# Kernel optimization log

Measured on AMD Instinct MI355X. Metric: run time of the kernel, lower is better.

The kernel has to match this reference:

```python
import jax, jax.numpy as jnp
import numpy as np

B = 1; C = 96; NH = 4; HD = 24; WIN = 3; LL = 27; SR = 8
Dd, Hh, Ww = 16, 40, 40
N = Dd * Hh * Ww
pH, pW, pD = Hh // SR, Ww // SR, Dd // SR
PL = pH * pW * pD
T = 4096


def _build_mask():
    p = WIN // 2
    m = np.zeros((Dd + 2 * p, Hh + 2 * p, Ww + 2 * p), bool)
    m[p:Dd + p, p:Hh + p, p:Ww + p] = True
    pats = np.stack([m[dz:dz + Dd, dy:dy + Hh, dx:dx + Ww]
                     for dz in range(WIN) for dy in range(WIN) for dx in range(WIN)], axis=-1)
    return jnp.asarray(~pats.reshape(N, LL))  # True where padded (masked)

MASK = _build_mask()


def _layernorm(x, w, b, eps=1e-5):
    mu = jnp.mean(x, axis=-1, keepdims=True)
    var = jnp.var(x, axis=-1, keepdims=True)
    return (x - mu) / jnp.sqrt(var + eps) * w + b


def _l2(x, eps=1e-12):
    n = jnp.sqrt(jnp.sum(x * x, axis=-1, keepdims=True))
    return x / jnp.maximum(n, eps)


def _unfold3d(x):
    # x: (B,C,D,H,W) -> (B,C,N,27), kernel order (kd,kh,kw) as torch unfold(2).unfold(3).unfold(4)
    p = WIN // 2
    xp = jnp.pad(x, ((0, 0), (0, 0), (p, p), (p, p), (p, p)))
    pats = [xp[:, :, dz:dz + Dd, dy:dy + Hh, dx:dx + Ww]
            for dz in range(WIN) for dy in range(WIN) for dx in range(WIN)]
    return jnp.stack(pats, axis=-1).reshape(x.shape[0], C, N, LL)


def _conv3(x, w):
    return jax.lax.conv_general_dilated(x, w, (1, 1, 1), 'SAME',
                                        dimension_numbers=('NCDHW', 'OIDHW', 'NCDHW'))


def _bn(x, p, eps=1e-5):
    sh = (1, C, 1, 1, 1)
    return (x - p[2].reshape(sh)) / jnp.sqrt(p[3].reshape(sh) + eps) * p[0].reshape(sh) + p[1].reshape(sh)


def _lrelu(x):
    return jnp.where(x >= 0, x, 0.01 * x)


def _resblock(x, w1, p1, w2, p2):
    h = _lrelu(_bn(_conv3(x, w1), p1))
    h = _bn(_conv3(h, w2), p2)
    return _lrelu(h + x)


def _forward(x, relative_pos_index, relative_coords_table, seq_length_scale,
             norm_w, norm_b, gamma, w_qkvv, temperature, temperature2, query_embedding,
             rel_bias_local, learnable_tokens, learnable_bias, sr_w, sr_b,
             epa_norm_w, epa_norm_b, w_kv, cpb1_w, cpb1_b, cpb2_w, cpb2_b,
             out1_w, out1_b, out2_w, out2_b,
             c51a_w, c51a_bn, c51b_w, c51b_bn, c52a_w, c52a_bn, c52b_w, c52b_bn,
             conv8_w, conv8_b):
    Bq = x.shape[0]
    # flatten (D,H,W) -> N tokens; pos_embed=True adds 1.0 (faithful to `x + True`)
    xt = x.reshape(Bq, C, N).transpose(0, 2, 1) + 1.0
    xn = _layernorm(xt, norm_w, norm_b)
    qkvv = (xn @ w_qkvv.T).reshape(Bq, N, 4, NH, HD).transpose(2, 0, 3, 1, 4)
    q, k, v_ca, v_sa = qkvv[0], qkvv[1], qkvv[2], qkvv[3]  # (B,NH,N,HD)
    qn = _l2(q)
    qs = (qn + query_embedding) * (jax.nn.softplus(temperature) * seq_length_scale)
    k_img = k.transpose(0, 1, 3, 2).reshape(Bq, C, Dd, Hh, Ww)
    v_img = v_sa.transpose(0, 1, 3, 2).reshape(Bq, C, Dd, Hh, Ww)
    k_loc = _unfold3d(k_img).reshape(Bq, NH, HD, N, LL).transpose(0, 1, 3, 2, 4)  # (B,NH,N,HD,LL)
    v_loc = _unfold3d(v_img).reshape(Bq, NH, HD, N, LL).transpose(0, 1, 3, 2, 4)
    a_loc = jnp.einsum('bhnd,bhndk->bhnk', qs, k_loc) + rel_bias_local[:, None, :]
    a_loc = jnp.where(MASK[None, None], -jnp.inf, a_loc)
    # pooled branch (note faithful (H,W,D) reshape as in source)
    xp = xn.transpose(0, 2, 1).reshape(Bq, C, Hh, Ww, Dd)
    xp = jax.nn.gelu(jnp.einsum('oc,bcxyz->boxyz', sr_w, xp)
                     + sr_b[None, :, None, None, None], approximate=False)
    xp = xp.reshape(Bq, C, pH, SR, pW, SR, pD, SR).mean(axis=(3, 5, 7))  # adaptive avg pool
    xp = xp.reshape(Bq, C, PL).transpose(0, 2, 1)
    xp = _layernorm(xp, epa_norm_w, epa_norm_b)
    kv = (xp @ w_kv.T).reshape(Bq, PL, 2 * NH, HD).transpose(0, 2, 1, 3)
    k_pool, v_pool = kv[:, :NH], kv[:, NH:]
    tab = jax.nn.relu(relative_coords_table @ cpb1_w.T + cpb1_b) @ cpb2_w.T + cpb2_b  # (T,NH)
    pool_bias = jnp.take(tab.T, relative_pos_index.reshape(-1), axis=1).reshape(NH, N, PL)
    a_pool = jnp.einsum('bhnd,bhpd->bhnp', qs, _l2(k_pool)) + pool_bias[None]
    attn = jax.nn.softmax(jnp.concatenate([a_loc, a_pool], axis=-1), axis=-1)
    a_loc, a_pool = attn[..., :LL], attn[..., LL:]
    a_loc = jnp.einsum('bhnd,hdk->bhnk', qn, learnable_tokens) + learnable_bias[None] + a_loc
    x_loc = jnp.einsum('bhnk,bhndk->bhnd', a_loc, v_loc)
    x_pool = jnp.einsum('bhnp,bhpd->bhnd', a_pool, v_pool)
    x_sa = (x_loc + x_pool).transpose(0, 2, 1, 3).reshape(Bq, N, C)
    # channel attention branch
    qt = _l2(q.transpose(0, 1, 3, 2))
    kt = _l2(k.transpose(0, 1, 3, 2))
    vt = v_ca.transpose(0, 1, 3, 2)
    a_ca = jax.nn.softmax(jnp.einsum('bhdn,bhen->bhde', qt, kt) * temperature2, axis=-1)
    x_ca = jnp.einsum('bhde,bhen->bhdn', a_ca, vt).transpose(0, 3, 1, 2).reshape(Bq, N, C)
    epa = jnp.concatenate([x_sa @ out1_w.T + out1_b, x_ca @ out2_w.T + out2_b], axis=-1)
    ax = xt + gamma * epa
    skip = ax.reshape(Bq, Hh, Ww, Dd, C).transpose(0, 4, 1, 2, 3)  # (B,C,H,W,D)
    h = _resblock(skip, c51a_w, c51a_bn, c51b_w, c51b_bn)
    h = _resblock(h, c52a_w, c52a_bn, c52b_w, c52b_bn)
    return skip + jnp.einsum('oc,bcxyz->boxyz', conv8_w, h) + conv8_b[None, :, None, None, None]


def setup_inputs():
    key = jax.random.key(0)
    ks = iter(jax.random.split(key, 64))
    r = lambda shape, s=0.02: jax.random.normal(next(ks), shape, jnp.float32) * s
    d = {}
    d['x'] = jax.random.normal(next(ks), (B, C, Dd, Hh, Ww), jnp.float32)
    d['relative_pos_index'] = jax.random.randint(next(ks), (N * PL,), 0, T, jnp.int32)
    d['relative_coords_table'] = jax.random.normal(next(ks), (T, 3), jnp.float32)
    d['seq_length_scale'] = jnp.ones((1,), jnp.float32)
    d['norm_w'] = 1.0 + r((C,)); d['norm_b'] = r((C,))
    d['gamma'] = jnp.full((C,), 0.01, jnp.float32)
    d['w_qkvv'] = r((4 * C, C))
    d['temperature'] = jnp.full((NH, 1, 1), float(np.log(np.exp(1 / 0.24) - 1)), jnp.float32)
    d['temperature2'] = jnp.ones((NH, 1, 1), jnp.float32)
    d['query_embedding'] = r((NH, 1, HD))
    d['rel_bias_local'] = r((NH, LL), 0.0004)
    d['learnable_tokens'] = r((NH, HD, LL))
    d['learnable_bias'] = jnp.zeros((NH, 1, LL), jnp.float32)
    d['sr_w'] = r((C, C)); d['sr_b'] = r((C,))
    d['epa_norm_w'] = 1.0 + r((C,)); d['epa_norm_b'] = r((C,))
    d['w_kv'] = r((2 * C, C))
    d['cpb1_w'] = r((512, 3)); d['cpb1_b'] = r((512,))
    d['cpb2_w'] = r((NH, 512)); d['cpb2_b'] = r((NH,))
    d['out1_w'] = r((C // 2, C)); d['out1_b'] = r((C // 2,))
    d['out2_w'] = r((C // 2, C)); d['out2_b'] = r((C // 2,))
    bn = lambda: jnp.stack([1.0 + r((C,)), r((C,)), jnp.zeros((C,), jnp.float32), jnp.ones((C,), jnp.float32)])
    d['c51a_w'] = r((C, C, 3, 3, 3)); d['c51a_bn'] = bn()
    d['c51b_w'] = r((C, C, 3, 3, 3)); d['c51b_bn'] = bn()
    d['c52a_w'] = r((C, C, 3, 3, 3)); d['c52a_bn'] = bn()
    d['c52b_w'] = r((C, C, 3, 3, 3)); d['c52b_bn'] = bn()
    d['conv8_w'] = r((C, C)); d['conv8_b'] = r((C,))
    return d


def reference(x, relative_pos_index, relative_coords_table, seq_length_scale,
              norm_w, norm_b, gamma, w_qkvv, temperature, temperature2, query_embedding,
              rel_bias_local, learnable_tokens, learnable_bias, sr_w, sr_b,
              epa_norm_w, epa_norm_b, w_kv, cpb1_w, cpb1_b, cpb2_w, cpb2_b,
              out1_w, out1_b, out2_w, out2_b,
              c51a_w, c51a_bn, c51b_w, c51b_bn, c52a_w, c52a_bn, c52b_w, c52b_bn,
              conv8_w, conv8_b):
    return _forward(x, relative_pos_index, relative_coords_table, seq_length_scale,
                    norm_w, norm_b, gamma, w_qkvv, temperature, temperature2, query_embedding,
                    rel_bias_local, learnable_tokens, learnable_bias, sr_w, sr_b,
                    epa_norm_w, epa_norm_b, w_kv, cpb1_w, cpb1_b, cpb2_w, cpb2_b,
                    out1_w, out1_b, out2_w, out2_b,
                    c51a_w, c51a_bn, c51b_w, c51b_bn, c52a_w, c52a_bn, c52b_w, c52b_bn,
                    conv8_w, conv8_b)
```

## Files before the change

kernel.cpp:

```cpp
#include <hip/hip_runtime.h>
#include <hip/hip_bf16.h>

#define NN 25600
#define CC 96
#define NHh 4
#define HDd 24
#define SSLOT 2457600
#define WP 269568

typedef unsigned short ushort_t;
typedef float f32x4 __attribute__((ext_vector_type(4)));
typedef short s16x8 __attribute__((ext_vector_type(8)));
typedef _Float16 f16;
typedef f16 h2v __attribute__((ext_vector_type(2)));

__device__ __forceinline__ float LD(const void* p, int i){
  return ((const float*)p)[i];
}
__device__ __forceinline__ float b2f(ushort_t u){ return __uint_as_float(((unsigned)u)<<16); }
__device__ __forceinline__ ushort_t f2b(float f){
  unsigned u = __float_as_uint(f);
  unsigned r = (u + 0x7fffu + ((u>>16)&1u))>>16;
  return (ushort_t)r;
}
__device__ __forceinline__ ushort_t f2h(float f){
  f16 hv = (f16)f;
  return *reinterpret_cast<ushort_t*>(&hv);
}
__device__ __forceinline__ float fdot2(h2v a, h2v b, float c){
#if __has_builtin(__builtin_amdgcn_fdot2)
  return __builtin_amdgcn_fdot2(a, b, c, false);
#else
  return c + (float)a[0]*(float)b[0] + (float)a[1]*(float)b[1];
#endif
}
__device__ __forceinline__ void gl_lds16(const void* g, const void* l){
  __builtin_amdgcn_global_load_lds(
      (const __attribute__((address_space(1))) unsigned*)g,
      (__attribute__((address_space(3))) unsigned*)l, 16, 0, 0);
}

#define NEGINF (-3.0e38f)

__global__ __launch_bounds__(256) void k_mega(
    const void* w0, const void* w1, const void* w2, const void* w3,
    const void* wq, const void* wsr, const void* w8,
    const void* o1w, const void* o1b, const void* o2w, const void* o2b,
    const void* b0, const void* b1, const void* b2bn, const void* b3,
    const void* ltok,
    ushort_t* __restrict__ WB2, ushort_t* __restrict__ WQH,
    ushort_t* __restrict__ WSH, ushort_t* __restrict__ W8H,
    ushort_t* __restrict__ WE, float* __restrict__ EB,
    float* __restrict__ BNS, ushort_t* __restrict__ LTOKT,
    float* __restrict__ ZB,
    const int* __restrict__ rpi, int* __restrict__ rpiT,
    const void* __restrict__ x, const void* __restrict__ nw,
    const void* __restrict__ nb, ushort_t* __restrict__ XNH,
    const void* __restrict__ rct, const void* __restrict__ w1t,
    const void* __restrict__ b1t, const void* __restrict__ w2t,
    const void* __restrict__ b2t, float* __restrict__ TAB)
{
  __shared__ __align__(16) char SMEM[15400];
  int b = blockIdx.x, tid = threadIdx.x;
  if(b < 4212){
    int e = b*256 + tid;
    {
      int t = e/WP, r = e%WP;
      int tap = r/9984, r2 = r%9984, o = r2/104, p = r2%104;
      const void* w = (t==0)? w0 : (t==1)? w1 : (t==2)? w2 : w3;
      WB2[e] = (p<96)? f2b(LD(w, (o*96+p)*27 + tap)) : (ushort_t)0;
    }
    if(e < 36864) WQH[e] = f2b(LD(wq,e));
    if(e < 9216){ WSH[e] = f2b(LD(wsr,e)); W8H[e] = f2b(LD(w8,e)); }
    if(e < 96*192){
      int o = e/192, c2 = e%192;
      float v = 0.f;
      if(o < 48 && c2 < 96)        v = LD(o1w, o*96 + c2);
      else if(o >= 48 && c2 >= 96) v = LD(o2w, (o-48)*96 + (c2-96));
      WE[e] = f2b(v);
      if(c2 == 0) EB[o] = (o<48)? LD(o1b,o) : LD(o2b,o-48);
    }
    if(e < 384){
      int t = e/96, o = e%96;
      const void* bn = (t==0)? b0 : (t==1)? b1 : (t==2)? b2bn : b3;
      float g=LD(bn,o), bb=LD(bn,96+o), mu=LD(bn,192+o), var=LD(bn,288+o);
      float s = g*rsqrtf(var+1e-5f);
      BNS[t*192+o] = s;
      BNS[t*192+96+o] = bb - mu*s;
    }
    if(e < 4096){
      int h = e/1024, r = e%1024, kk = r/32, d = r%32;
      float v = (d<24 && kk<27)? LD(ltok, (h*24+d)*27 + kk) : 0.f;
      LTOKT[e] = f2b(v);
    }
    if(e < 8) ZB[e] = 0.f;
  } else if(b < 4612){
    int* T = (int*)SMEM;
    int n0 = (b-4212)*64;
    for(int f=tid; f<3200; f+=256){
      int nl = f/50, p = f%50;
      T[p*65+nl] = rpi[n0*50 + f];
    }
    __syncthreads();
    for(int f=tid; f<3200; f+=256){
      int p = f>>6, nl = f&63;
      rpiT[(size_t)p*NN + n0 + nl] = T[p*65+nl];
    }
  } else if(b < 5012){
    float* reds  = (float*)SMEM;
    float* redss = reds + 256;
    ushort_t* OUT = (ushort_t*)(redss + 256);
    int bx = b - 4612;
    int nl = tid&63, cg = tid>>6;
    int n = bx*64 + nl;
    float v[24]; float s=0.f, ss=0.f;
    #pragma unroll
    for(int i=0;i<24;i++){
      float t = LD(x, (cg*24+i)*NN + n) + 1.0f;
      v[i]=t; s+=t; ss+=t*t;
    }
    reds[cg*64+nl]=s; redss[cg*64+nl]=ss;
    __syncthreads();
    float S  = reds[nl]+reds[64+nl]+reds[128+nl]+reds[192+nl];
    float SS = redss[nl]+redss[64+nl]+redss[128+nl]+redss[192+nl];
    float mu = S*(1.0f/CC);
    float inv = rsqrtf(SS*(1.0f/CC) - mu*mu + 1e-5f);
    #pragma unroll
    for(int i=0;i<24;i++){
      int c = cg*24+i;
      OUT[nl*100+c] = f2b((v[i]-mu)*inv*LD(nw,c) + LD(nb,c));
    }
    __syncthreads();
    for(int f=tid; f<3072; f+=256){
      int r = f/48, dp = f%48;
      unsigned pk = (unsigned)OUT[r*100+dp*2] | ((unsigned)OUT[r*100+dp*2+1]<<16);
      *reinterpret_cast<unsigned*>(XNH + (size_t)(bx*64+r)*96 + dp*2) = pk;
    }
  } else {
    float* red = (float*)SMEM;
    int tt = b - 5012, j = tid;
    float r0=LD(rct,tt*3), r1=LD(rct,tt*3+1), r2=LD(rct,tt*3+2);
    float hA = r0*LD(w1t,j*3) + r1*LD(w1t,j*3+1) + r2*LD(w1t,j*3+2) + LD(b1t,j);
    hA = fmaxf(hA, 0.f);
    int j2 = j + 256;
    float hB = r0*LD(w1t,j2*3) + r1*LD(w1t,j2*3+1) + r2*LD(w1t,j2*3+2) + LD(b1t,j2);
    hB = fmaxf(hB, 0.f);
    int lane=j&63, wid=j>>6;
    for(int h=0;h<4;h++){
      float v = hA*LD(w2t, h*512+j) + hB*LD(w2t, h*512+j2);
      #pragma unroll
      for(int off=32;off;off>>=1) v += __shfl_down(v, off);
      if(lane==0) red[wid*4+h]=v;
    }
    __syncthreads();
    if(j<4){
      float s = red[j] + red[4+j] + red[8+j] + red[12+j];
      TAB[tt*4+j] = s + LD(b2t,j);
    }
  }
}

__global__ __launch_bounds__(256,2) void k_qkvsr(
    const ushort_t* __restrict__ XNH, const ushort_t* __restrict__ WQH,
    const ushort_t* __restrict__ WSH, const void* __restrict__ srb,
    float* __restrict__ out, ushort_t* __restrict__ KH,
    ushort_t* __restrict__ VH, float* __restrict__ XP2){
  int tid=threadIdx.x, w=tid>>6, lane=tid&63, lan=lane&15, grp=lane>>4;
  int n = blockIdx.x*64 + w*16 + lan;
  const ushort_t* bp = XNH + n*96;
  if(blockIdx.y < 2){
    int ybase = blockIdx.y*192;
    f32x4 acc[12];
    #pragma unroll
    for(int mt=0;mt<12;mt++) acc[mt] = (f32x4)(0.f);
    #pragma unroll
    for(int s=0;s<3;s++){
      s16x8 b = *reinterpret_cast<const s16x8*>(bp + s*32 + grp*8);
      #pragma unroll
      for(int mt=0;mt<12;mt++){
        s16x8 a = *reinterpret_cast<const s16x8*>(WQH + (ybase+mt*16+lan)*96 + s*32 + grp*8);
        acc[mt] = __builtin_amdgcn_mfma_f32_16x16x32_bf16(a, b, acc[mt], 0,0,0);
      }
    }
    #pragma unroll
    for(int mt=0;mt<12;mt++){
      int o0 = ybase + mt*16 + grp*4;
      int sl = o0/96, rr = o0%96, h = rr/24, dd = rr%24;
      f32x4 v = acc[mt];
      if(sl == 3){
        ushort4 pk = { f2h(v[0]), f2h(v[1]), f2h(v[2]), f2h(v[3]) };
        *reinterpret_cast<ushort4*>(VH + ((size_t)h*NN+n)*24 + dd) = pk;
      } else {
        *reinterpret_cast<float4*>(out + sl*SSLOT + ((size_t)h*NN+n)*24 + dd) =
            (float4){v[0],v[1],v[2],v[3]};
        if(sl == 1){
          ushort4 pk = { f2h(v[0]), f2h(v[1]), f2h(v[2]), f2h(v[3]) };
          *reinterpret_cast<ushort4*>(KH + ((size_t)h*NN+n)*24 + dd) = pk;
        }
      }
    }
  } else {
    f32x4 acc[6];
    #pragma unroll
    for(int mt=0;mt<6;mt++) acc[mt] = (f32x4)(0.f);
    #pragma unroll
    for(int s=0;s<3;s++){
      s16x8 b = *reinterpret_cast<const s16x8*>(bp + s*32 + grp*8);
      #pragma unroll
      for(int mt=0;mt<6;mt++){
        s16x8 a = *reinterpret_cast<const s16x8*>(WSH + (mt*16+lan)*96 + s*32 + grp*8);
        acc[mt] = __builtin_amdgcn_mfma_f32_16x16x32_bf16(a, b, acc[mt], 0,0,0);
      }
    }
    #pragma unroll
    for(int mt=0;mt<6;mt++){
      #pragma unroll
      for(int r=0;r<4;r++){
        int o = mt*16 + grp*4 + r;
        float y = acc[mt][r] + LD(srb,o);
        y = 0.5f*y*(1.0f + erff(y*0.70710678118f));
        XP2[o*NN+n] = y;
      }
    }
  }
}

__global__ __launch_bounds__(256) void k_mid1(
    const float* __restrict__ Q, const void* __restrict__ temp,
    const void* __restrict__ sls, const void* __restrict__ qe,
    const ushort_t* __restrict__ LTOKT, const void* __restrict__ lbias,
    float* __restrict__ QS, ushort_t* __restrict__ LTH,
    const float* __restrict__ XP2, float* __restrict__ pooled)
{
  __shared__ ushort_t QL[4][64][32];
  int b = blockIdx.x, tid = threadIdx.x;
  if(b < 400){
    int h = tid>>6, nl = tid&63;
    int n0 = b*64, n = n0 + nl;
    const float* qr = Q + ((size_t)h*NN+n)*24;
    float qv[24]; float ssum=0.f;
    #pragma unroll
    for(int d=0;d<24;d++){ qv[d]=qr[d]; ssum+=qv[d]*qv[d]; }
    float inv = 1.0f/fmaxf(sqrtf(ssum), 1e-12f);
    float t = LD(temp,h);
    float sp = log1pf(expf(t)) * LD(sls,0);
    float* qs = QS + ((size_t)h*NN+n)*24;
    #pragma unroll
    for(int d=0;d<24;d+=2){
      float q0 = qv[d]*inv, q1 = qv[d+1]*inv;
      unsigned pk = (unsigned)f2b(q0) | ((unsigned)f2b(q1)<<16);
      *reinterpret_cast<unsigned*>(&QL[h][nl][d]) = pk;
      qs[d]   = (q0 + LD(qe, h*24+d))*sp;
      qs[d+1] = (q1 + LD(qe, h*24+d+1))*sp;
    }
    *reinterpret_cast<unsigned*>(&QL[h][nl][24]) = 0;
    *reinterpret_cast<unsigned*>(&QL[h][nl][26]) = 0;
    *reinterpret_cast<unsigned*>(&QL[h][nl][28]) = 0;
    *reinterpret_cast<unsigned*>(&QL[h][nl][30]) = 0;
    __syncthreads();
    int lane=tid&63, lan=lane&15, grp=lane>>4;
    f32x4 acc[4][2];
    #pragma unroll
    for(int j=0;j<4;j++)
      #pragma unroll
      for(int tt=0;tt<2;tt++) acc[j][tt] = (f32x4)(0.f);
    #pragma unroll
    for(int j=0;j<4;j++){
      s16x8 bb = *reinterpret_cast<const s16x8*>(&QL[h][j*16+lan][grp*8]);
      #pragma unroll
      for(int tt=0;tt<2;tt++){
        s16x8 a = *reinterpret_cast<const s16x8*>(LTOKT + h*1024 + (tt*16+lan)*32 + grp*8);
        acc[j][tt] = __builtin_amdgcn_mfma_f32_16x16x32_bf16(a, bb, acc[j][tt], 0,0,0);
      }
    }
    #pragma unroll
    for(int j=0;j<4;j++){
      int nn = n0 + j*16 + lan;
      #pragma unroll
      for(int tt=0;tt<2;tt++){
        int k0 = tt*16 + grp*4;
        if(k0 < 28){
          ushort4 pk;
          ushort_t* pp = reinterpret_cast<ushort_t*>(&pk);
          #pragma unroll
          for(int r=0;r<4;r++){
            int k = k0+r;
            float v = acc[j][tt][r] + ((k<27)? LD(lbias, h*27+k) : 0.f);
            pp[r] = f2h(v);
          }
          *reinterpret_cast<ushort4*>(LTH + ((size_t)h*NN+nn)*28 + k0) = pk;
        }
      }
    }
  } else {
    int w = tid>>6, lane = tid&63;
    int pb = (b-400)*4 + w;
    int c = pb % CC, p = pb / CC;
    int ph = p/10, pw = (p%10)/2, pd = p%2;
    float s = 0.f;
    for(int t=lane; t<512; t+=64){
      int i=t>>6, j=(t>>3)&7, k=t&7;
      int m = (ph*8+i)*640 + (pw*8+j)*16 + (pd*8+k);
      s += XP2[c*NN+m];
    }
    #pragma unroll
    for(int off=32;off;off>>=1) s += __shfl_down(s, off);
    if(lane==0) pooled[p*CC+c] = s*(1.0f/512.0f);
  }
}

__global__ void k_mid2(const float* __restrict__ pooled, const void* __restrict__ ew,
                       const void* __restrict__ eb, const void* __restrict__ wkv,
                       ushort_t* __restrict__ KPNH, ushort_t* __restrict__ VPH){
  __shared__ float row[96], lnr[96], st[2], kk[96];
  int p = blockIdx.x, t = threadIdx.x;
  if(t<96) row[t] = pooled[p*96+t];
  __syncthreads();
  if(t==0){
    float s=0.f, ss=0.f;
    for(int c=0;c<96;c++){ float v=row[c]; s+=v; ss+=v*v; }
    float mu=s*(1.0f/96.0f);
    float var=ss*(1.0f/96.0f)-mu*mu;
    st[0]=mu; st[1]=rsqrtf(var+1e-5f);
  }
  __syncthreads();
  if(t<96) lnr[t] = (row[t]-st[0])*st[1]*LD(ew,t) + LD(eb,t);
  __syncthreads();
  if(t<192){
    float a=0.f;
    for(int c=0;c<96;c++) a += LD(wkv, t*96+c)*lnr[c];
    int g=t/24, d=t%24;
    if(g<4) kk[t]=a;
    else    VPH[((g-4)*50+p)*24+d] = f2h(a);
  }
  __syncthreads();
  if(t<96){
    int g=t/24, d=t%24;
    float ss=0.f;
    #pragma unroll
    for(int e=0;e<24;e++){ float v=kk[g*24+e]; ss+=v*v; }
    float inv = 1.0f/fmaxf(sqrtf(ss),1e-12f);
    KPNH[((g*50+p)*24)+d] = f2h(kk[t]*inv);
  }
}

__global__ __launch_bounds__(512) void k_big(
    const float* __restrict__ QS, const ushort_t* __restrict__ KH,
    const ushort_t* __restrict__ VH,
    const ushort_t* __restrict__ KPNH, const ushort_t* __restrict__ VPH,
    const float* __restrict__ TAB, const int* __restrict__ rpiT,
    const void* __restrict__ rbl, const ushort_t* __restrict__ LTH,
    ushort_t* __restrict__ XH,
    const float* __restrict__ Q, const float* __restrict__ K,
    float* __restrict__ PAR)
{
  __shared__ ushort_t KVH[2][600*26];
  int bb = blockIdx.x, tid = threadIdx.x;
  if(bb < 400){
    int tile = bb % 100, h = bb / 100;
    int g = tile/25, sp = tile%25, hg = sp/5, wg = sp%5;
    int role = tid>>8, q = tid & 255;
    int wq = q>>6, l = q&63;
    int hy = l>>3, wx = l&7;
    int d0 = g*4 + wq;
    int h0 = hg*8+hy, w0 = wg*8+wx;
    int n = d0*1600 + h0*40 + w0;

    const ushort_t* KHh = KH + (size_t)h*NN*24;
    const ushort_t* VHh = VH + (size_t)h*NN*24;
    for(int f=tid; f<3600; f+=512){
      int t = f/1800, rem = f%1800, row = rem/3, qq = rem%3;
      int dr = row/100, yr = (row%100)/10, xr = row%10;
      int zc = min(max(g*4+dr-1,0),15), yc = min(max(hg*8+yr-1,0),39), xc = min(max(wg*8+xr-1,0),39);
      const ushort_t* src = (t? VHh : KHh) + (size_t)(zc*1600+yc*40+xc)*24 + qq*8;
      const unsigned* s32 = reinterpret_cast<const unsigned*>(src);
      unsigned a0=s32[0], a1=s32[1], a2=s32[2], a3=s32[3];
      unsigned* d32 = reinterpret_cast<unsigned*>(&KVH[t][row*26 + qq*8]);
      d32[0]=a0; d32[1]=a1; d32[2]=a2; d32[3]=a3;
    }

    h2v qp[12];
    {
      const float* qsp = QS + ((size_t)h*NN+n)*24;
      #pragma unroll
      for(int d=0; d<24; d+=4){
        float4 a = *reinterpret_cast<const float4*>(qsp+d);
        qp[d/2]   = (h2v){ (f16)a.x, (f16)a.y };
        qp[d/2+1] = (h2v){ (f16)a.z, (f16)a.w };
      }
    }
    __syncthreads();

    float m_r, s_r;
    h2v accA[12], accT[12];
    #pragma unroll
    for(int j=0;j<12;j++){ accA[j]=(h2v){(f16)0.f,(f16)0.f}; accT[j]=(h2v){(f16)0.f,(f16)0.f}; }

    const h2v* kph = reinterpret_cast<const h2v*>(KPNH) + (size_t)h*50*12;
    const h2v* vph = reinterpret_cast<const h2v*>(VPH)  + (size_t)h*50*12;

    if(role==0){
      float av[39]; unsigned okm=0;
      #pragma unroll
      for(int k=0;k<27;k++){
        int kz=k/9, ky=(k%9)/3, kx=k%3;
        bool ok = (unsigned)(d0+kz-1)<16u && (unsigned)(h0+ky-1)<40u && (unsigned)(w0+kx-1)<40u;
        float sc = NEGINF;
        if(ok){
          okm |= 1u<<k;
          const h2v* kr = reinterpret_cast<const h2v*>(
              &KVH[0][((wq+kz)*100 + (hy+ky)*10 + (wx+kx))*26]);
          sc = LD(rbl, h*27+k);
          #pragma unroll
          for(int j=0;j<12;j++) sc = fdot2(kr[j], qp[j], sc);
        }
        av[k]=sc;
      }
      #pragma unroll
      for(int p=0;p<12;p++){
        float sc = TAB[rpiT[(size_t)p*NN+n]*4 + h];
        const h2v* kr = kph + p*12;
        #pragma unroll
        for(int j=0;j<12;j++) sc = fdot2(kr[j], qp[j], sc);
        av[27+p]=sc;
      }
      float m = av[0];
      #pragma unroll
      for(int k=1;k<39;k++) m = fmaxf(m, av[k]);
      const f16* ltp = reinterpret_cast<const f16*>(LTH) + ((size_t)h*NN+n)*28;
      float s = 0.f;
      #pragma unroll
      for(int k=0;k<27;k++){
        if(okm>>k & 1u){
          int kz=k/9, ky=(k%9)/3, kx=k%3;
          float e = __expf(av[k]-m);
          s += e;
          float ltv = (float)ltp[k];
          h2v we = { (f16)e, (f16)e };
          h2v wt = { (f16)ltv, (f16)ltv };
          const h2v* vr = reinterpret_cast<const h2v*>(
              &KVH[1][((wq+kz)*100 + (hy+ky)*10 + (wx+kx))*26]);
          #pragma unroll
          for(int j=0;j<12;j++){
            accA[j] = vr[j]*we + accA[j];
            accT[j] = vr[j]*wt + accT[j];
          }
        }
      }
      #pragma unroll
      for(int p=0;p<12;p++){
        float e = __expf(av[27+p]-m);
        s += e;
        h2v we = { (f16)e, (f16)e };
        const h2v* vr = vph + p*12;
        #pragma unroll
        for(int j=0;j<12;j++) accA[j] = vr[j]*we + accA[j];
      }
      m_r = m; s_r = s;
    } else {
      float av[38];
      #pragma unroll
      for(int p=0;p<38;p++){
        int pp = p+12;
        float sc = TAB[rpiT[(size_t)pp*NN+n]*4 + h];
        const h2v* kr = kph + pp*12;
        #pragma unroll
        for(int j=0;j<12;j++) sc = fdot2(kr[j], qp[j], sc);
        av[p]=sc;
      }
      float m = av[0];
      #pragma unroll
      for(int p=1;p<38;p++) m = fmaxf(m, av[p]);
      float s = 0.f;
      #pragma unroll
      for(int p=0;p<38;p++){
        float e = __expf(av[p]-m);
        s += e;
        h2v we = { (f16)e, (f16)e };
        const h2v* vr = vph + (p+12)*12;
        #pragma unroll
        for(int j=0;j<12;j++) accA[j] = vr[j]*we + accA[j];
      }
      m_r = m; s_r = s;
    }
    __syncthreads();

    float* PP = (float*)&KVH[0][0];
    if(role==1){
      PP[q*15+0] = m_r;
      PP[q*15+1] = s_r;
      #pragma unroll
      for(int j=0;j<12;j++){
        h2v a = accA[j];
        PP[q*15+2+j] = __uint_as_float(*reinterpret_cast<unsigned*>(&a));
      }
    }
    __syncthreads();

    float* TRF = (float*)&KVH[0][0] + 4096;
    if(role==0){
      float mp = PP[q*15+0], sp2 = PP[q*15+1];
      float m = fmaxf(m_r, mp);
      float a = __expf(m_r - m), b = __expf(mp - m);
      float inv = 1.0f/(a*s_r + b*sp2);
      #pragma unroll
      for(int j=0;j<12;j++){
        unsigned pb = __float_as_uint(PP[q*15+2+j]);
        h2v ap = *reinterpret_cast<h2v*>(&pb);
        float v0 = (a*(float)accA[j][0] + b*(float)ap[0])*inv + (float)accT[j][0];
        float v1 = (a*(float)accA[j][1] + b*(float)ap[1])*inv + (float)accT[j][1];
        TRF[q*25 + 2*j]   = v0;
        TRF[q*25 + 2*j+1] = v1;
      }
    }
    __syncthreads();

    for(int f=tid; f<3072; f+=512){
      int q2 = f/12, dp = f%12;
      int w2 = q2>>6, l2 = q2&63;
      int n2 = (g*4+w2)*1600 + (hg*8+(l2>>3))*40 + (wg*8+(l2&7));
      float v0 = TRF[q2*25+dp*2], v1 = TRF[q2*25+dp*2+1];
      unsigned pk = (unsigned)f2b(v0) | ((unsigned)f2b(v1)<<16);
      *reinterpret_cast<unsigned*>(XH + (size_t)n2*192 + h*24 + dp*2) = pk;
    }
  } else {
    float* red = (float*)&KVH[0][0];
    int b2 = bb - 400;
    int hd = b2 % 96, chunk = b2 / 96;
    int h = hd/24, d = hd%24;
    int n0 = chunk*3200;
    float acc[24]; float qss=0.f, kss=0.f;
    #pragma unroll
    for(int e=0;e<24;e++) acc[e]=0.f;
    for(int i=tid; i<3200; i+=512){
      int n = n0 + i;
      const float4* kr4 = reinterpret_cast<const float4*>(K + ((size_t)h*NN+n)*24);
      float4 k0=kr4[0], k1=kr4[1], k2=kr4[2], k3=kr4[3], k4=kr4[4], k5=kr4[5];
      float qv = Q[((size_t)h*NN+n)*24+d];
      qss += qv*qv;
      float kd = LD(K, ((size_t)h*NN+n)*24+d);
      kss += kd*kd;
      acc[0]+=qv*k0.x; acc[1]+=qv*k0.y; acc[2]+=qv*k0.z; acc[3]+=qv*k0.w;
      acc[4]+=qv*k1.x; acc[5]+=qv*k1.y; acc[6]+=qv*k1.z; acc[7]+=qv*k1.w;
      acc[8]+=qv*k2.x; acc[9]+=qv*k2.y; acc[10]+=qv*k2.z; acc[11]+=qv*k2.w;
      acc[12]+=qv*k3.x; acc[13]+=qv*k3.y; acc[14]+=qv*k3.z; acc[15]+=qv*k3.w;
      acc[16]+=qv*k4.x; acc[17]+=qv*k4.y; acc[18]+=qv*k4.z; acc[19]+=qv*k4.w;
      acc[20]+=qv*k5.x; acc[21]+=qv*k5.y; acc[22]+=qv*k5.z; acc[23]+=qv*k5.w;
    }
    int lane=tid&63, wid=tid>>6;
    #pragma unroll
    for(int j=0;j<26;j++){
      float v = (j<24)? acc[j] : (j==24? qss : kss);
      #pragma unroll
      for(int off=32;off;off>>=1) v += __shfl_down(v, off);
      if(lane==0) red[wid*26+j]=v;
    }
    __syncthreads();
    if(tid<26){
      int j=tid;
      float s = 0.f;
      #pragma unroll
      for(int w8c=0;w8c<8;w8c++) s += red[w8c*26+j];
      PAR[((size_t)chunk*96+hd)*26 + j] = s;
    }
  }
}

__global__ __launch_bounds__(256) void k_caep(
    const float* __restrict__ PAR, const void* __restrict__ t2,
    const float* __restrict__ VCA, ushort_t* __restrict__ XH){
  __shared__ float A[2304];
  __shared__ float kinv_s[96];
  int t = threadIdx.x;
  float S[24]; float qi=0.f;
  int hh = (t<96)? t/24 : 0;
  if(t<96){
    float qss=0.f, kss=0.f;
    #pragma unroll
    for(int e=0;e<24;e++) S[e]=0.f;
    for(int c=0;c<8;c++){
      const float* pp = PAR + ((size_t)c*96+t)*26;
      #pragma unroll
      for(int e=0;e<24;e++) S[e] += pp[e];
      qss += pp[24]; kss += pp[25];
    }
    qi = 1.0f/fmaxf(sqrtf(qss),1e-12f);
    kinv_s[t] = 1.0f/fmaxf(sqrtf(kss),1e-12f);
  }
  __syncthreads();
  if(t<96){
    float tv = LD(t2,hh);
    float v[24]; float m = NEGINF;
    #pragma unroll
    for(int e=0;e<24;e++){
      v[e] = S[e]*qi*kinv_s[hh*24+e]*tv;
      m = fmaxf(m, v[e]);
    }
    float s=0.f;
    #pragma unroll
    for(int e=0;e<24;e++){ v[e]=__expf(v[e]-m); s+=v[e]; }
    float inv=1.0f/s;
    #pragma unroll
    for(int e=0;e<24;e++) A[t*24+e] = v[e]*inv;
  }
  __syncthreads();
  int h = t>>6, l = t&63;
  int n = blockIdx.x*64 + l;
  float vr[24];
  const float* vp = VCA + ((size_t)h*NN+n)*24;
  #pragma unroll
  for(int e=0;e<24;e+=4){
    float4 v = *reinterpret_cast<const float4*>(vp+e);
    vr[e]=v.x; vr[e+1]=v.y; vr[e+2]=v.z; vr[e+3]=v.w;
  }
  float o[24];
  #pragma unroll
  for(int d=0;d<24;d++){
    float a=0.f;
    const float* ar = A + (h*24+d)*24;
    #pragma unroll
    for(int e=0;e<24;e++) a += ar[e]*vr[e];
    o[d]=a;
  }
  #pragma unroll
  for(int d=0;d<24;d+=2){
    unsigned pk = (unsigned)f2b(o[d]) | ((unsigned)f2b(o[d+1])<<16);
    *reinterpret_cast<unsigned*>(XH + (size_t)n*192 + 96 + h*24 + d) = pk;
  }
}

__global__ __launch_bounds__(256,2) void k_epam(
    const ushort_t* __restrict__ XH, const ushort_t* __restrict__ WE,
    const float* __restrict__ EB, const void* __restrict__ x,
    const void* __restrict__ gamma,
    float* __restrict__ SKIPF, ushort_t* __restrict__ SKIPH){
  int tid=threadIdx.x, w=tid>>6, lane=tid&63, lan=lane&15, grp=lane>>4;
  int n = blockIdx.x*64 + w*16 + lan;
  const ushort_t* bp = XH + (size_t)n*192;
  f32x4 acc[6];
  #pragma unroll
  for(int mt=0;mt<6;mt++) acc[mt] = (f32x4)(0.f);
  #pragma unroll
  for(int s=0;s<6;s++){
    s16x8 b = *reinterpret_cast<const s16x8*>(bp + s*32 + grp*8);
    #pragma unroll
    for(int mt=0;mt<6;mt++){
      s16x8 a = *reinterpret_cast<const s16x8*>(WE + (mt*16+lan)*192 + s*32 + grp*8);
      acc[mt] = __builtin_amdgcn_mfma_f32_16x16x32_bf16(a, b, acc[mt], 0,0,0);
    }
  }
  #pragma unroll
  for(int mt=0;mt<6;mt++){
    #pragma unroll
    for(int r=0;r<4;r++){
      int o = mt*16 + grp*4 + r;
      float e = acc[mt][r] + EB[o];
      float v = LD(x, o*NN+n) + 1.0f + LD(gamma,o)*e;
      SKIPF[(size_t)n*96+o] = v;
      SKIPH[(size_t)n*96+o] = f2b(v);
    }
  }
}

__global__ __launch_bounds__(256,2) void k_convm8(
    const ushort_t* __restrict__ IN, const ushort_t* __restrict__ WB2,
    const float* __restrict__ BNS, const float* __restrict__ resf,
    const float* __restrict__ ZB,
    ushort_t* __restrict__ outh, float* __restrict__ outf)
{
  __shared__ ushort_t BUF[2][16640];
  int tid = threadIdx.x;
  int w = tid>>6, lane = tid&63;
  int lan = lane&15, grp = lane>>4;
  int bs = (blockIdx.x&7)*50 + (blockIdx.x>>3);
  int n0 = bs*64;

  auto STAGE = [&](int tap, ushort_t* buf){
    int dx=tap/9-1, dy=(tap%9)/3-1, dz=tap%3-1;
    int off = dx*640 + dy*16 + dz;
    const ushort_t* wsrc = WB2 + tap*9984;
    #pragma unroll
    for(int i=0;i<9;i++){
      int cb = i*256 + w*64;
      if(cb >= 2080) break;
      int c = cb + lane;
      const void* src;
      if(c < 1248){
        src = wsrc + c*8;
      } else {
        int c2 = c - 1248;
        int r = c2/13, p = c2%13;
        int nn = n0 + r;
        int X = nn/640, rr2 = nn%640, Y = rr2/16, Z = nn&15;
        bool ok = (p<12) && (unsigned)(X+dx)<40u && (unsigned)(Y+dy)<40u && (unsigned)(Z+dz)<16u;
        src = ok ? (const void*)(IN + (size_t)(nn+off)*96 + p*8) : (const void*)ZB;
      }
      if(c < 2080) gl_lds16(src, buf + cb*8);
    }
  };

  f32x4 acc[6];
  #pragma unroll
  for(int mt=0;mt<6;mt++) acc[mt] = (f32x4)(0.f);

  STAGE(0, BUF[0]);
  asm volatile("s_waitcnt vmcnt(0)" ::: "memory");
  __builtin_amdgcn_s_barrier();

  for(int tap=0; tap<27; ++tap){
    if(tap<26){
      STAGE(tap+1, BUF[(tap+1)&1]);
      asm volatile("s_waitcnt vmcnt(8)" ::: "memory");
    } else {
      asm volatile("s_waitcnt vmcnt(0)" ::: "memory");
    }
    __builtin_amdgcn_s_barrier();
    __builtin_amdgcn_sched_barrier(0);
    const ushort_t* Ab = BUF[tap&1];
    const ushort_t* Bb = Ab + 9984;
    s16x8 bfr[3];
    #pragma unroll
    for(int s=0;s<3;s++)
      bfr[s] = *reinterpret_cast<const s16x8*>(Bb + (w*16+lan)*104 + s*32 + grp*8);
    #pragma unroll
    for(int mt=0;mt<6;mt++){
      #pragma unroll
      for(int s=0;s<3;s++){
        s16x8 a = *reinterpret_cast<const s16x8*>(Ab + (mt*16+lan)*104 + s*32 + grp*8);
        acc[mt] = __builtin_amdgcn_mfma_f32_16x16x32_bf16(a, bfr[s], acc[mt], 0,0,0);
      }
    }
    __builtin_amdgcn_s_barrier();
  }

  float* TR = (float*)&BUF[0][0];
  int nl = w*16 + lan;
  #pragma unroll
  for(int mt=0;mt<6;mt++){
    int ob = mt*16 + grp*4;
    float4 vv;
    vv.x = acc[mt][0]*BNS[ob+0] + BNS[96+ob+0];
    vv.y = acc[mt][1]*BNS[ob+1] + BNS[96+ob+1];
    vv.z = acc[mt][2]*BNS[ob+2] + BNS[96+ob+2];
    vv.w = acc[mt][3]*BNS[ob+3] + BNS[96+ob+3];
    *reinterpret_cast<float4*>(TR + nl*100 + ob) = vv;
  }
  __syncthreads();
  for(int f=tid; f<3072; f+=256){
    int r = f/48, cp = f%48;
    int n = n0 + r;
    float v0 = TR[r*100+cp*2], v1 = TR[r*100+cp*2+1];
    if(resf){ v0 += resf[(size_t)n*96+cp*2]; v1 += resf[(size_t)n*96+cp*2+1]; }
    v0 = (v0>=0.f)? v0 : 0.01f*v0;
    v1 = (v1>=0.f)? v1 : 0.01f*v1;
    unsigned pk = (unsigned)f2b(v0) | ((unsigned)f2b(v1)<<16);
    *reinterpret_cast<unsigned*>(outh + (size_t)n*96 + cp*2) = pk;
    if(outf){
      float2 fo; fo.x=v0; fo.y=v1;
      *reinterpret_cast<float2*>(outf + (size_t)n*96 + cp*2) = fo;
    }
  }
}

__global__ __launch_bounds__(256,2) void k_finm(
    const float* __restrict__ SKIPF, const ushort_t* __restrict__ T3H,
    const ushort_t* __restrict__ W8H, const void* __restrict__ b,
    float* __restrict__ out){
  int tid=threadIdx.x, w=tid>>6, lane=tid&63, lan=lane&15, grp=lane>>4;
  int n = blockIdx.x*64 + w*16 + lan;
  const ushort_t* bp = T3H + n*96;
  f32x4 acc[6];
  #pragma unroll
  for(int mt=0;mt<6;mt++) acc[mt] = (f32x4)(0.f);
  #pragma unroll
  for(int s=0;s<3;s++){
    s16x8 bb = *reinterpret_cast<const s16x8*>(bp + s*32 + grp*8);
    #pragma unroll
    for(int mt=0;mt<6;mt++){
      s16x8 a = *reinterpret_cast<const s16x8*>(W8H + (mt*16+lan)*96 + s*32 + grp*8);
      acc[mt] = __builtin_amdgcn_mfma_f32_16x16x32_bf16(a, bb, acc[mt], 0,0,0);
    }
  }
  #pragma unroll
  for(int mt=0;mt<6;mt++){
    #pragma unroll
    for(int r=0;r<4;r++){
      int o = mt*16 + grp*4 + r;
      out[o*NN+n] = SKIPF[(size_t)n*96+o] + acc[mt][r] + LD(b,o);
    }
  }
}

extern "C" void kernel_launch(void* const* d_in, const int* in_sizes, int n_in,
                              void* d_out, int out_size, void* d_ws, size_t ws_size,
                              hipStream_t stream){
  const void* x     = d_in[0];
  const int*  rpi   = (const int*)d_in[1];
  const void* rct   = d_in[2];
  const void* sls   = d_in[3];
  const void* nw    = d_in[4];
  const void* nb    = d_in[5];
  const void* gamma = d_in[6];
  const void* wqkvv = d_in[7];
  const void* temp  = d_in[8];
  const void* temp2 = d_in[9];
  const void* qe    = d_in[10];
  const void* rbl   = d_in[11];
  const void* ltok  = d_in[12];
  const void* lbias = d_in[13];
  const void* srw   = d_in[14];
  const void* srb   = d_in[15];
  const void* epaw  = d_in[16];
  const void* epab  = d_in[17];
  const void* wkv   = d_in[18];
  const void* c1w   = d_in[19];
  const void* c1b   = d_in[20];
  const void* c2w   = d_in[21];
  const void* c2b   = d_in[22];
  const void* o1w   = d_in[23];
  const void* o1b   = d_in[24];
  const void* o2w   = d_in[25];
  const void* o2b   = d_in[26];
  const void* w51a  = d_in[27];
  const void* bn51a = d_in[28];
  const void* w51b  = d_in[29];
  const void* bn51b = d_in[30];
  const void* w52a  = d_in[31];
  const void* bn52a = d_in[32];
  const void* w52b  = d_in[33];
  const void* bn52b = d_in[34];
  const void* w8    = d_in[35];
  const void* b8    = d_in[36];

  float* ws = (float*)d_ws;
  const size_t S = SSLOT;
  ushort_t* XNH = (ushort_t*)ws;
  float* SKIPF = ws;
  float* Q     = ws + 1*S;
  float* Kb    = ws + 2*S;
  float* T2F   = ws + 2*S;
  float* VCA   = ws + 3*S;
  ushort_t* KH = (ushort_t*)(ws + 4*S);
  ushort_t* VH = KH + SSLOT;
  float* QS    = ws + 6*S;
  ushort_t* XH = (ushort_t*)(ws + 7*S);
  int*   rpiT  = (int*)(ws + 8*S);
  float* XP2   = ws + 7*S;
  ushort_t* SKIPH = (ushort_t*)(ws + 4*S);
  ushort_t* T1H   = SKIPH + SSLOT;
  ushort_t* T2H   = (ushort_t*)(ws + 5*S);
  ushort_t* T3H   = T2H + SSLOT;
  float* SM  = ws + 9*S;
  float* pooled = SM;
  float* TAB    = SM + 19200;
  ushort_t* WB2 = (ushort_t*)(SM + 40960);
  float* BNS    = SM + 40960 + 539136;
  ushort_t* WQH = (ushort_t*)(BNS + 768);
  ushort_t* WSH = WQH + 36864;
  ushort_t* W8H = WSH + 9216;
  ushort_t* WE  = W8H + 9216;
  float* EB     = BNS + 768 + 18432 + 4608 + 4608 + 9216;
  float* PAR    = EB + 96;
  ushort_t* KPNH = (ushort_t*)(PAR + 19968);
  ushort_t* VPH  = KPNH + 4800;
  ushort_t* LTOKT= VPH + 4800;
  ushort_t* LTH  = LTOKT + 4096;
  float* ZB      = (float*)(LTH + 2867200);

  k_mega  <<<9108, 256, 0, stream>>>(w51a, w51b, w52a, w52b, wqkvv, srw, w8,
                                     o1w, o1b, o2w, o2b,
                                     bn51a, bn51b, bn52a, bn52b, ltok,
                                     WB2, WQH, WSH, W8H, WE, EB, BNS, LTOKT, ZB,
                                     rpi, rpiT,
                                     x, nw, nb, XNH,
                                     rct, c1w, c1b, c2w, c2b, TAB);
  k_qkvsr <<<dim3(400,3), 256, 0, stream>>>(XNH, WQH, WSH, srb, Q, KH, VH, XP2);
  k_mid1  <<<1600, 256, 0, stream>>>(Q, temp, sls, qe, LTOKT, lbias, QS, LTH,
                                     XP2, pooled);
  k_mid2  <<<50,   256, 0, stream>>>(pooled, epaw, epab, wkv, KPNH, VPH);
  k_big   <<<1168, 512, 0, stream>>>(QS, KH, VH, KPNH, VPH, TAB, rpiT,
                                     rbl, LTH, XH, Q, Kb, PAR);
  k_caep  <<<400,  256, 0, stream>>>(PAR, temp2, VCA, XH);
  k_epam  <<<400,  256, 0, stream>>>(XH, WE, EB, x, gamma, SKIPF, SKIPH);
  k_convm8<<<400, 256, 0, stream>>>(SKIPH, WB2,        BNS,     nullptr, ZB, T1H, nullptr);
  k_convm8<<<400, 256, 0, stream>>>(T1H,   WB2+WP,     BNS+192, SKIPF,   ZB, T2H, T2F);
  k_convm8<<<400, 256, 0, stream>>>(T2H,   WB2+2*WP,   BNS+384, nullptr, ZB, T1H, nullptr);
  k_convm8<<<400, 256, 0, stream>>>(T1H,   WB2+3*WP,   BNS+576, T2F,     ZB, T3H, nullptr);
  k_finm  <<<400, 256, 0, stream>>>(SKIPF, T3H, W8H, b8, (float*)d_out);
}
```

Measured before the change: 303.1 us.

## Compute channel-attention Q·Kᵀ partials with register-tiled 4x4 outer products per head

The channel-attention branch of k_big used one block per (head, dim, chunk) and reloaded the full K row for every query dimension, which gave 768 blocks with heavy redundant K reads. It now uses one block per (head, chunk). Each wave covers 400 tokens, and 36 lanes each accumulate a 4x4 tile of the 24x24 Gram matrix plus the squared norms, followed by a shared-memory reduction across waves. This cuts the grid from 1168 to 432 blocks and greatly reduces global loads. The cost is that 28 of the 64 lanes in each wave sit idle and fewer blocks are available for parallelism.

```diff
diff --git a/kernel.cpp b/kernel.cpp
--- a/kernel.cpp
+++ b/kernel.cpp
@@ -524,44 +524,66 @@
       *reinterpret_cast<unsigned*>(XH + (size_t)n2*192 + h*24 + dp*2) = pk;
     }
   } else {
-    float* red = (float*)&KVH[0][0];
+    float* WRED = (float*)&KVH[0][0];
     int b2 = bb - 400;
-    int hd = b2 % 96, chunk = b2 / 96;
-    int h = hd/24, d = hd%24;
-    int n0 = chunk*3200;
-    float acc[24]; float qss=0.f, kss=0.f;
-    #pragma unroll
-    for(int e=0;e<24;e++) acc[e]=0.f;
-    for(int i=tid; i<3200; i+=512){
-      int n = n0 + i;
-      const float4* kr4 = reinterpret_cast<const float4*>(K + ((size_t)h*NN+n)*24);
-      float4 k0=kr4[0], k1=kr4[1], k2=kr4[2], k3=kr4[3], k4=kr4[4], k5=kr4[5];
-      float qv = Q[((size_t)h*NN+n)*24+d];
-      qss += qv*qv;
-      float kd = LD(K, ((size_t)h*NN+n)*24+d);
-      kss += kd*kd;
-      acc[0]+=qv*k0.x; acc[1]+=qv*k0.y; acc[2]+=qv*k0.z; acc[3]+=qv*k0.w;
-      acc[4]+=qv*k1.x; acc[5]+=qv*k1.y; acc[6]+=qv*k1.z; acc[7]+=qv*k1.w;
-      acc[8]+=qv*k2.x; acc[9]+=qv*k2.y; acc[10]+=qv*k2.z; acc[11]+=qv*k2.w;
-      acc[12]+=qv*k3.x; acc[13]+=qv*k3.y; acc[14]+=qv*k3.z; acc[15]+=qv*k3.w;
-      acc[16]+=qv*k4.x; acc[17]+=qv*k4.y; acc[18]+=qv*k4.z; acc[19]+=qv*k4.w;
-      acc[20]+=qv*k5.x; acc[21]+=qv*k5.y; acc[22]+=qv*k5.z; acc[23]+=qv*k5.w;
-    }
-    int lane=tid&63, wid=tid>>6;
-    #pragma unroll
-    for(int j=0;j<26;j++){
-      float v = (j<24)? acc[j] : (j==24? qss : kss);
-      #pragma unroll
-      for(int off=32;off;off>>=1) v += __shfl_down(v, off);
-      if(lane==0) red[wid*26+j]=v;
+    int h = b2 >> 3, chunk = b2 & 7;
+    int wv = tid >> 6, lane = tid & 63;
+    int n0 = chunk*3200 + wv*400;
+    const float* Qh = Q + (size_t)h*NN*24;
+    const float* Kh = K + (size_t)h*NN*24;
+    int r = lane/6, cgl = lane%6;
+    bool act = lane < 36;
+    int d1 = r*4, d2 = cgl*4;
+    float accm[4][4];
+    #pragma unroll
+    for(int i=0;i<4;i++)
+      #pragma unroll
+      for(int j=0;j<4;j++) accm[i][j]=0.f;
+    float qss4[4] = {0.f,0.f,0.f,0.f}, kss4[4] = {0.f,0.f,0.f,0.f};
+    if(act){
+      #pragma unroll 4
+      for(int i=0;i<400;i++){
+        int n = n0 + i;
+        float4 q4 = *reinterpret_cast<const float4*>(Qh + (size_t)n*24 + d1);
+        float4 k4 = *reinterpret_cast<const float4*>(Kh + (size_t)n*24 + d2);
+        float qa[4] = {q4.x,q4.y,q4.z,q4.w};
+        float ka[4] = {k4.x,k4.y,k4.z,k4.w};
+        #pragma unroll
+        for(int i2=0;i2<4;i2++)
+          #pragma unroll
+          for(int j=0;j<4;j++) accm[i2][j] += qa[i2]*ka[j];
+        #pragma unroll
+        for(int e=0;e<4;e++){ qss4[e]+=qa[e]*qa[e]; kss4[e]+=ka[e]*ka[e]; }
+      }
+      float* wp = WRED + (wv*36 + lane)*25;
+      #pragma unroll
+      for(int i=0;i<4;i++)
+        #pragma unroll
+        for(int j=0;j<4;j++) wp[i*4+j] = accm[i][j];
+      if(r == cgl){
+        #pragma unroll
+        for(int e=0;e<4;e++){ wp[16+e]=qss4[e]; wp[20+e]=kss4[e]; }
+      }
     }
     __syncthreads();
-    if(tid<26){
-      int j=tid;
+    for(int c=tid; c<624; c+=512){
       float s = 0.f;
-      #pragma unroll
-      for(int w8c=0;w8c<8;w8c++) s += red[w8c*26+j];
-      PAR[((size_t)chunk*96+hd)*26 + j] = s;
+      if(c < 576){
+        int d1o = c/24, d2o = c%24;
+        int li = (d1o>>2)*6 + (d2o>>2);
+        int sl = (d1o&3)*4 + (d2o&3);
+        #pragma unroll
+        for(int w8=0;w8<8;w8++) s += WRED[(w8*36+li)*25+sl];
+        PAR[((size_t)chunk*96 + h*24 + d1o)*26 + d2o] = s;
+      } else {
+        int cc = c - 576;
+        int d = cc % 24, isk = cc / 24;
+        int li = (d>>2)*7;
+        int sl = 16 + isk*4 + (d&3);
+        #pragma unroll
+        for(int w8=0;w8<8;w8++) s += WRED[(w8*36+li)*25+sl];
+        PAR[((size_t)chunk*96 + h*24 + d)*26 + 24 + isk] = s;
+      }
     }
   }
 }
@@ -878,7 +900,7 @@
   k_mid1  <<<1600, 256, 0, stream>>>(Q, temp, sls, qe, LTOKT, lbias, QS, LTH,
                                      XP2, pooled);
   k_mid2  <<<50,   256, 0, stream>>>(pooled, epaw, epab, wkv, KPNH, VPH);
-  k_big   <<<1168, 512, 0, stream>>>(QS, KH, VH, KPNH, VPH, TAB, rpiT,
+  k_big   <<<432,  512, 0, stream>>>(QS, KH, VH, KPNH, VPH, TAB, rpiT,
                                      rbl, LTH, XH, Q, Kb, PAR);
   k_caep  <<<400,  256, 0, stream>>>(PAR, temp2, VCA, XH);
   k_epam  <<<400,  256, 0, stream>>>(XH, WE, EB, x, gamma, SKIPF, SKIPH);
```

New measurement: 300.2 us. About the same (-0.9%).
